# Kernel optimization log

Measured on AMD Instinct MI355X. Metric: run time of the kernel, lower is better.

Reference implementation:

```python
import jax, jax.numpy as jnp
import numpy as np
from math import sqrt

B, S, D, H = 4, 2048, 1024, 16
HD = D // H


def setup_inputs() -> dict:
    key = jax.random.key(0)
    ks = jax.random.split(key, 16)
    w = 0.02
    q = jax.random.normal(ks[0], (B, S, D), jnp.float32)
    k = jax.random.normal(ks[1], (B, S, D), jnp.float32)
    v = jax.random.normal(ks[2], (B, S, D), jnp.float32)
    # causal attention mask [1,1,S,S]
    attn_mask = jnp.tril(jnp.ones((S, S), jnp.int32))[None, None]
    # padding mask [B,1,1,S]; force position 0 valid so no softmax row is all -inf
    pad_mask = jax.random.randint(ks[3], (B, 1, 1, S), 0, 2, jnp.int32)
    pad_mask = pad_mask.at[..., 0].set(1)
    params = {
        'Wq': jax.random.normal(ks[4], (D, D), jnp.float32) * w,
        'bq': jnp.zeros((D,), jnp.float32),
        'Wk': jax.random.normal(ks[5], (D, D), jnp.float32) * w,
        'bk': jnp.zeros((D,), jnp.float32),
        'Wv': jax.random.normal(ks[6], (D, D), jnp.float32) * w,
        'bv': jnp.zeros((D,), jnp.float32),
        'Wo': jax.random.normal(ks[7], (D, D), jnp.float32) * w,
        'bo': jnp.zeros((D,), jnp.float32),
        'gamma': jnp.ones((D,), jnp.float32),
        'beta': jnp.zeros((D,), jnp.float32),
    }
    return dict(q=q, k=k, v=v, attn_mask=attn_mask, pad_mask=pad_mask, **params)


def _mha(q, k, v, Wq, bq, Wk, bk, Wv, bv, Wo, bo, gamma, beta, attn_mask, pad_mask):
    seq = q.shape[1]
    # residual path is detached in the original (q.clone().detach())
    x = jax.lax.stop_gradient(q)
    # Linear projections (torch Linear: y = x @ W.T + b)
    qp = (q @ Wq.T + bq).reshape(-1, H, seq, HD)   # raw view, NO head transpose (faithful)
    kp = (k @ Wk.T + bk).reshape(-1, H, seq, HD)
    vp = (v @ Wv.T + bv).reshape(-1, H, seq, HD)
    scores = jnp.einsum('bhqd,bhkd->bhqk', qp, kp)   # [B,H,S,S]
    scores = jnp.where(pad_mask == 0, -jnp.inf, scores)
    scores = jnp.where(attn_mask == 0, -jnp.inf, scores)
    # scaling applied AFTER masking, as in source
    attn = jax.nn.softmax(scores / sqrt(HD), axis=-1)
    out = jnp.einsum('bhqk,bhkd->bhqd', attn, vp).reshape(-1, seq, D)
    out = out @ Wo.T + bo  # dropout is identity in eval
    y = x + out
    mean = jnp.mean(y, axis=-1, keepdims=True)
    std = jnp.sqrt(jnp.mean((y - mean) ** 2, axis=-1, keepdims=True))
    return gamma * ((y - mean) / (std + 1e-8)) + beta


def reference(q, k, v, attn_mask, pad_mask, Wq, bq, Wk, bk, Wv, bv, Wo, bo, gamma, beta):
    return _mha(q, k, v, Wq, bq, Wk, bk, Wv, bv, Wo, bo, gamma, beta, attn_mask, pad_mask)
```

## Files before the change

kernel.cpp:

```cpp
#include <hip/hip_runtime.h>
#include <hip/hip_bf16.h>
#include <math.h>

#define B_  4
#define S_  2048
#define D_  1024
#define H_  16
#define HD_ 64
#define SD_  (S_*D_)
#define SHD_ (S_*HD_)

typedef __attribute__((ext_vector_type(8))) short          bf16x8;
typedef __attribute__((ext_vector_type(4))) float          f32x4;
typedef __attribute__((ext_vector_type(8))) unsigned short us8;
typedef __attribute__((ext_vector_type(4))) unsigned short us4;

__device__ __forceinline__ unsigned short f2bf(float x) {
  unsigned int u = __float_as_uint(x);
  u += 0x7fffu + ((u >> 16) & 1u);
  return (unsigned short)(u >> 16);
}
__device__ __forceinline__ float bf2f(unsigned short u) {
  return __uint_as_float(((unsigned int)u) << 16);
}

__device__ __forceinline__ void gload16(const unsigned short* g, unsigned short* l) {
  __builtin_amdgcn_global_load_lds(
      (const __attribute__((address_space(1))) unsigned int*)g,
      (__attribute__((address_space(3))) unsigned int*)l,
      16, 0, 0);
}

__device__ __forceinline__ void stage_swz(const unsigned short* __restrict__ g,
                                          int rstride ,
                                          unsigned short* lds, int tid)
{
#pragma unroll
  for (int rr = 0; rr < 2; ++rr) {
    const int cidx = tid + rr * 256;
    const int row  = cidx >> 3;
    const int sb   = ((cidx & 7) * 16) ^ ((row & 7) << 4);
    gload16(g + (size_t)row * rstride + (sb >> 1), lds + cidx * 8);
  }
}

__device__ __forceinline__ void read_frag_pair(const unsigned short* lds, int row,
                                               int quad, bf16x8& f0, bf16x8& f1)
{
  const int sw = (row & 7) << 4;
  const unsigned short* p = lds + row * 64;
  f0 = *(const bf16x8*)(p + (((quad * 16) ^ sw) >> 1));
  f1 = *(const bf16x8*)(p + (((64 + quad * 16) ^ sw) >> 1));
}

__global__ __launch_bounds__(256) void cvt_a(const float* __restrict__ s,
                                             unsigned short* __restrict__ d)
{
  int i = blockIdx.x * 256 + threadIdx.x;
  float4 v = ((const float4*)s)[i];
  us4 o = { f2bf(v.x), f2bf(v.y), f2bf(v.z), f2bf(v.w) };
  *(us4*)(d + (size_t)i * 4) = o;
}

__global__ __launch_bounds__(256) void cvt_w(const float* __restrict__ w0,
                                             const float* __restrict__ w1,
                                             const float* __restrict__ w2,
                                             const float* __restrict__ w3,
                                             unsigned short* __restrict__ dst)
{
  const float* s = (blockIdx.y == 0) ? w0 : (blockIdx.y == 1) ? w1
                 : (blockIdx.y == 2) ? w2 : w3;
  unsigned short* d = dst + (size_t)blockIdx.y * 1024 * 1024;
  int i = blockIdx.x * 256 + threadIdx.x;
  float4 v = ((const float4*)s)[i];
  us4 o = { f2bf(v.x), f2bf(v.y), f2bf(v.z), f2bf(v.w) };
  *(us4*)(d + (size_t)i * 4) = o;
}

__global__ __launch_bounds__(256) void pad_cvt(const int* __restrict__ pad,
                                               float* __restrict__ padf)
{
  int i = (blockIdx.x * 256 + threadIdx.x) * 4;
  int4 pv = *(const int4*)(pad + i);
  float4 o = { pv.x ? 0.f : -1e30f, pv.y ? 0.f : -1e30f,
               pv.z ? 0.f : -1e30f, pv.w ? 0.f : -1e30f };
  *(float4*)(padf + i) = o;
}

__global__ __launch_bounds__(256) void cvt_all(
    const float* __restrict__ q, const float* __restrict__ k,
    const float* __restrict__ v,
    const float* __restrict__ w0, const float* __restrict__ w1,
    const float* __restrict__ w2, const float* __restrict__ w3,
    const int* __restrict__ pad,
    unsigned short* __restrict__ Ac3, unsigned short* __restrict__ Wall,
    float* __restrict__ padf)
{
  const int bx = blockIdx.x;
  if (bx < 24576) {
    const int y = bx >> 13;
    const int i = (bx & 8191) * 256 + threadIdx.x;
    const float* s = (y == 0) ? q : (y == 1) ? k : v;
    unsigned short* d = Ac3 + (size_t)y * (B_ * (size_t)SD_);
    float4 x = ((const float4*)s)[i];
    us4 o = { f2bf(x.x), f2bf(x.y), f2bf(x.z), f2bf(x.w) };
    *(us4*)(d + (size_t)i * 4) = o;
  } else if (bx < 24576 + 4096) {
    const int bw = bx - 24576;
    const int y = bw >> 10;
    const int i = (bw & 1023) * 256 + threadIdx.x;
    const float* s = (y == 0) ? w0 : (y == 1) ? w1 : (y == 2) ? w2 : w3;
    unsigned short* d = Wall + (size_t)y * 1024 * 1024;
    float4 x = ((const float4*)s)[i];
    us4 o = { f2bf(x.x), f2bf(x.y), f2bf(x.z), f2bf(x.w) };
    *(us4*)(d + (size_t)i * 4) = o;
  } else {
    const int i = ((bx - 28672) * 256 + threadIdx.x) * 4;
    int4 pv = *(const int4*)(pad + i);
    float4 o = { pv.x ? 0.f : -1e30f, pv.y ? 0.f : -1e30f,
                 pv.z ? 0.f : -1e30f, pv.w ? 0.f : -1e30f };
    *(float4*)(padf + i) = o;
  }
}

__device__ __forceinline__ void gemm_body(
    const unsigned short* __restrict__ A,
    const unsigned short* __restrict__ Wb,
    const float* __restrict__ bias,
    unsigned short* __restrict__ Cb,
    int n0, int m0)
{
  __shared__ unsigned short As[2][128 * 32];
  __shared__ unsigned short Bs[2][128 * 32];

  const int tid  = threadIdx.x;
  const int lane = tid & 63;
  const int w    = tid >> 6;
  const int wm   = w >> 1, wn = w & 1;
  const int l16  = lane & 15, quad = lane >> 4;

  f32x4 acc[4][4];
#pragma unroll
  for (int mt = 0; mt < 4; ++mt)
#pragma unroll
    for (int nt = 0; nt < 4; ++nt) acc[mt][nt] = (f32x4){0.f, 0.f, 0.f, 0.f};

  const int srow = lane >> 2;
  const int sseg = (lane & 3) * 8;
  const int r0   = w * 32 + srow;

  const unsigned short* Ar0 = A  + (size_t)(m0 + r0) * 1024 + sseg;
  const unsigned short* Ar1 = A  + (size_t)(m0 + r0 + 16) * 1024 + sseg;
  const unsigned short* Br0 = Wb + (size_t)(n0 + r0) * 1024 + sseg;
  const unsigned short* Br1 = Wb + (size_t)(n0 + r0 + 16) * 1024 + sseg;

  auto STAGE = [&](int buf, int kt) {
    const int ko = kt * 32;
    gload16(Ar0 + ko, &As[buf][r0 * 32 + sseg]);
    gload16(Ar1 + ko, &As[buf][(r0 + 16) * 32 + sseg]);
    gload16(Br0 + ko, &Bs[buf][r0 * 32 + sseg]);
    gload16(Br1 + ko, &Bs[buf][(r0 + 16) * 32 + sseg]);
  };

  STAGE(0, 0);
  int cur = 0;
  for (int kt = 0; kt < 32; ++kt) {
    if (kt < 31) {
      STAGE(cur ^ 1, kt + 1);
      asm volatile("s_waitcnt vmcnt(4)" ::: "memory");
    } else {
      asm volatile("s_waitcnt vmcnt(0)" ::: "memory");
    }
    __builtin_amdgcn_sched_barrier(0);
    __builtin_amdgcn_s_barrier();

    bf16x8 af[4], bfr[4];
#pragma unroll
    for (int mt = 0; mt < 4; ++mt)
      af[mt] = *(const bf16x8*)&As[cur][(wm * 64 + mt * 16 + l16) * 32 + quad * 8];
#pragma unroll
    for (int nt = 0; nt < 4; ++nt)
      bfr[nt] = *(const bf16x8*)&Bs[cur][(wn * 64 + nt * 16 + l16) * 32 + quad * 8];
#pragma unroll
    for (int mt = 0; mt < 4; ++mt)
#pragma unroll
      for (int nt = 0; nt < 4; ++nt)
        acc[mt][nt] = __builtin_amdgcn_mfma_f32_16x16x32_bf16(
            af[mt], bfr[nt], acc[mt][nt], 0, 0, 0);

    __builtin_amdgcn_sched_barrier(0);
    __builtin_amdgcn_s_barrier();
    cur ^= 1;
  }

#pragma unroll
  for (int nt = 0; nt < 4; ++nt) {
    const int ncol = n0 + wn * 64 + nt * 16 + l16;
    const float bv = bias[ncol];
#pragma unroll
    for (int mt = 0; mt < 4; ++mt) {
      const int row = m0 + wm * 64 + mt * 16 + quad * 4;
#pragma unroll
      for (int reg = 0; reg < 4; ++reg)
        Cb[(size_t)(row + reg) * 1024 + ncol] = f2bf(acc[mt][nt][reg] + bv);
    }
  }
}

__device__ __forceinline__ void xcd_coords(int& n0, int& m0)
{
  const int nwgx = gridDim.x;
  const int nwg  = nwgx * gridDim.y;
  const int bid  = blockIdx.y * nwgx + blockIdx.x;
  const int sw   = (bid & 7) * (nwg >> 3) + (bid >> 3);
  n0 = (sw % nwgx) * 128;
  m0 = (sw / nwgx) * 128;
}

__global__ __launch_bounds__(256) void gemm_mfma(
    const unsigned short* __restrict__ A, const unsigned short* __restrict__ Wb,
    const float* __restrict__ bias, unsigned short* __restrict__ Cb)
{
  int n0, m0;
  xcd_coords(n0, m0);
  gemm_body(A, Wb, bias, Cb, n0, m0);
}

__global__ __launch_bounds__(256) void gemm_qkv(
    const unsigned short* __restrict__ A3,
    const unsigned short* __restrict__ Wall,
    const float* __restrict__ bq, const float* __restrict__ bk,
    const float* __restrict__ bv,
    unsigned short* __restrict__ Qb, unsigned short* __restrict__ Kb,
    unsigned short* __restrict__ Vb)
{
  const int z = blockIdx.z;
  const unsigned short* A  = A3 + (size_t)z * (B_ * (size_t)SD_);
  const unsigned short* Wb = Wall + (size_t)z * 1024 * 1024;
  const float* bias = (z == 0) ? bq : (z == 1) ? bk : bv;
  unsigned short* Cb = (z == 0) ? Qb : (z == 1) ? Kb : Vb;
  int n0, m0;
  xcd_coords(n0, m0);
  gemm_body(A, Wb, bias, Cb, n0, m0);
}

__global__ __launch_bounds__(256) void vtrans(
    const unsigned short* __restrict__ V, unsigned short* __restrict__ Vt)
{
  __shared__ unsigned short t[64][72];
  const int tid = threadIdx.x;
  const int st  = blockIdx.x;
  const int bh  = blockIdx.y;
  const unsigned short* src = V + (size_t)bh * SHD_ + (size_t)st * 4096;

#pragma unroll
  for (int u = tid; u < 512; u += 256) {
    us8 vv = ((const us8*)src)[u];
    int s  = u >> 3;
    int dg = (u & 7) * 8;
    *(us8*)&t[s][dg] = vv;
  }
  __syncthreads();

  unsigned short* dst = Vt + (size_t)bh * SHD_ + st * 64;
#pragma unroll
  for (int u = tid; u < 1024; u += 256) {
    int d  = u >> 4;
    int s4 = (u & 15) * 4;
    us4 o = { t[s4][d], t[s4 + 1][d], t[s4 + 2][d], t[s4 + 3][d] };
    *(us4*)(dst + (size_t)d * 2048 + s4) = o;
  }
}

__global__ __launch_bounds__(256, 4) void attn_mfma(
    unsigned short* __restrict__ Qb, const unsigned short* __restrict__ Kb,
    const unsigned short* __restrict__ Vt, const float* __restrict__ padf)
{
  __shared__ unsigned short Ks[64 * 64];
  __shared__ unsigned short Vs[2][64 * 64];
  __shared__ unsigned short Ps[4][16][72];

  const int tid  = threadIdx.x;
  const int lane = tid & 63;
  const int w    = tid >> 6;
  const int p    = blockIdx.x;
  const int bh   = blockIdx.y;
  const int b    = bh >> 4;
  const size_t base = (size_t)bh * SHD_;

  const int l16  = lane & 15;
  const int quad = lane >> 4;

  for (int half = 0; half < 2; ++half) {
    const int it = half ? (31 - p) : p;

    bf16x8 qfrag[2];
    {
      const unsigned short* qrow = Qb + base + (size_t)(it * 64 + w * 16 + l16) * 64;
      qfrag[0] = *(const bf16x8*)(qrow + quad * 8);
      qfrag[1] = *(const bf16x8*)(qrow + 32 + quad * 8);
    }

    f32x4 oacc[4];
#pragma unroll
    for (int dt = 0; dt < 4; ++dt) oacc[dt] = (f32x4){0.f, 0.f, 0.f, 0.f};
    float mS = -INFINITY, lS = 0.f;

    __syncthreads();
    stage_swz(Kb + base, 64, Ks, tid);
    stage_swz(Vt + base, 2048, Vs[0], tid);
    float4 pf[4];
#pragma unroll
    for (int ct = 0; ct < 4; ++ct)
      pf[ct] = *(const float4*)(padf + b * S_ + ct * 16 + quad * 4);
    int cur = 0;

    for (int jt = 0; jt <= it; ++jt) {
      __syncthreads();

      f32x4 sacc[4];
#pragma unroll
      for (int ct = 0; ct < 4; ++ct) {
        bf16x8 k0, k1;
        read_frag_pair(Ks, ct * 16 + l16, quad, k0, k1);
        f32x4 s = (f32x4){0.f, 0.f, 0.f, 0.f};
        s = __builtin_amdgcn_mfma_f32_16x16x32_bf16(k0, qfrag[0], s, 0, 0, 0);
        s = __builtin_amdgcn_mfma_f32_16x16x32_bf16(k1, qfrag[1], s, 0, 0, 0);
        sacc[ct] = s;
      }

      float4 pfn[4];
      if (jt < it) {
        __syncthreads();
        stage_swz(Kb + base + (size_t)(jt + 1) * 4096, 64, Ks, tid);
        stage_swz(Vt + base + (jt + 1) * 64, 2048, Vs[cur ^ 1], tid);
#pragma unroll
        for (int ct = 0; ct < 4; ++ct)
          pfn[ct] = *(const float4*)(padf + b * S_ + (jt + 1) * 64 + ct * 16 + quad * 4);
      }

      float lg[4][4];
      float mx = -INFINITY;
#pragma unroll
      for (int ct = 0; ct < 4; ++ct)
#pragma unroll
        for (int reg = 0; reg < 4; ++reg) {
          float sc = fmaf(sacc[ct][reg], 0.125f, ((const float*)&pf[ct])[reg]);
          if (jt == it) {
            bool ok = (ct * 16 + quad * 4 + reg) <= (w * 16 + l16);
            sc = ok ? sc : -1e30f;
          }
          lg[ct][reg] = sc;
          mx = fmaxf(mx, sc);
        }
      mx = fmaxf(mx, __shfl_xor(mx, 16, 64));
      mx = fmaxf(mx, __shfl_xor(mx, 32, 64));
      const float mnew = fmaxf(mS, mx);
      const float a    = __expf(mS - mnew);
      float sm = 0.f;
#pragma unroll
      for (int ct = 0; ct < 4; ++ct) {
        us4 pk;
#pragma unroll
        for (int reg = 0; reg < 4; ++reg) {
          float pe = __expf(lg[ct][reg] - mnew);
          sm += pe;
          pk[reg] = f2bf(pe);
        }
        *(us4*)&Ps[w][l16][ct * 16 + quad * 4] = pk;
      }
      sm += __shfl_xor(sm, 16, 64);
      sm += __shfl_xor(sm, 32, 64);
      lS = lS * a + sm;
      mS = mnew;

      float aO[4];
#pragma unroll
      for (int reg = 0; reg < 4; ++reg) aO[reg] = __shfl(a, quad * 4 + reg, 64);
#pragma unroll
      for (int dt = 0; dt < 4; ++dt)
#pragma unroll
        for (int reg = 0; reg < 4; ++reg) oacc[dt][reg] *= aO[reg];

      bf16x8 pfrag0 = *(const bf16x8*)&Ps[w][l16][quad * 8];
      bf16x8 pfrag1 = *(const bf16x8*)&Ps[w][l16][32 + quad * 8];
#pragma unroll
      for (int dt = 0; dt < 4; ++dt) {
        bf16x8 v0, v1;
        read_frag_pair(Vs[cur], dt * 16 + l16, quad, v0, v1);
        oacc[dt] = __builtin_amdgcn_mfma_f32_16x16x32_bf16(pfrag0, v0, oacc[dt], 0, 0, 0);
        oacc[dt] = __builtin_amdgcn_mfma_f32_16x16x32_bf16(pfrag1, v1, oacc[dt], 0, 0, 0);
      }

      if (jt < it) {
#pragma unroll
        for (int ct = 0; ct < 4; ++ct) pf[ct] = pfn[ct];
        cur ^= 1;
      }
    }

    float lO[4];
#pragma unroll
    for (int reg = 0; reg < 4; ++reg) lO[reg] = __shfl(lS, quad * 4 + reg, 64);
#pragma unroll
    for (int reg = 0; reg < 4; ++reg) {
      const float rl = 1.0f / lO[reg];
      unsigned short* orow = Qb + base + (size_t)(it * 64 + w * 16 + quad * 4 + reg) * 64;
#pragma unroll
      for (int dt = 0; dt < 4; ++dt)
        orow[dt * 16 + l16] = f2bf(oacc[dt][reg] * rl);
    }
  }
}

__global__ __launch_bounds__(256) void ln_kernel(
    const float* __restrict__ x, const unsigned short* __restrict__ O,
    const float* __restrict__ gamma, const float* __restrict__ beta,
    float* __restrict__ out)
{
  __shared__ float red[8];
  const int row = blockIdx.x;
  const int tid = threadIdx.x;
  float4 xv = ((const float4*)x)[(size_t)row * 256 + tid];
  us4 ov4 = *(const us4*)(O + (size_t)row * 1024 + tid * 4);
  float4 y = make_float4(xv.x + bf2f(ov4[0]), xv.y + bf2f(ov4[1]),
                         xv.z + bf2f(ov4[2]), xv.w + bf2f(ov4[3]));
  float s1 = y.x + y.y + y.z + y.w;
  float s2 = y.x*y.x + y.y*y.y + y.z*y.z + y.w*y.w;
#pragma unroll
  for (int off = 32; off >= 1; off >>= 1) {
    s1 += __shfl_xor(s1, off, 64);
    s2 += __shfl_xor(s2, off, 64);
  }
  if ((tid & 63) == 0) { red[tid >> 6] = s1; red[4 + (tid >> 6)] = s2; }
  __syncthreads();
  s1 = red[0] + red[1] + red[2] + red[3];
  s2 = red[4] + red[5] + red[6] + red[7];
  const float mean = s1 * (1.0f / 1024.0f);
  const float var  = fmaxf(s2 * (1.0f / 1024.0f) - mean * mean, 0.f);
  const float rstd = 1.0f / (sqrtf(var) + 1e-8f);
  float4 gv = ((const float4*)gamma)[tid];
  float4 bv = ((const float4*)beta)[tid];
  float4 r;
  r.x = gv.x * (y.x - mean) * rstd + bv.x;
  r.y = gv.y * (y.y - mean) * rstd + bv.y;
  r.z = gv.z * (y.z - mean) * rstd + bv.z;
  r.w = gv.w * (y.w - mean) * rstd + bv.w;
  ((float4*)out)[(size_t)row * 256 + tid] = r;
}

extern "C" void kernel_launch(void* const* d_in, const int* in_sizes, int n_in,
                              void* d_out, int out_size, void* d_ws, size_t ws_size,
                              hipStream_t stream)
{
  const float* q  = (const float*)d_in[0];
  const float* k  = (const float*)d_in[1];
  const float* v  = (const float*)d_in[2];
  const int*   pad = (const int*)d_in[4];
  const float* Wq = (const float*)d_in[5];
  const float* bq = (const float*)d_in[6];
  const float* Wk = (const float*)d_in[7];
  const float* bk = (const float*)d_in[8];
  const float* Wv = (const float*)d_in[9];
  const float* bv = (const float*)d_in[10];
  const float* Wo = (const float*)d_in[11];
  const float* bo = (const float*)d_in[12];
  const float* gamma = (const float*)d_in[13];
  const float* beta  = (const float*)d_in[14];
  float* out = (float*)d_out;

  char* ws = (char*)d_ws;
  const size_t MB = 1024 * 1024;
  dim3 gg(8, 64), bb(256);

  if (ws_size >= 121 * MB) {
    unsigned short* Ac3  = (unsigned short*)(ws);
    unsigned short* Qb   = (unsigned short*)(ws + 48 * MB);
    unsigned short* Kb   = (unsigned short*)(ws + 64 * MB);
    unsigned short* Vb   = (unsigned short*)(ws + 80 * MB);
    unsigned short* Vtb  = (unsigned short*)(ws + 96 * MB);
    unsigned short* Wall = (unsigned short*)(ws + 112 * MB);
    float*          padf = (float*)(ws + 120 * MB);
    unsigned short* Obuf = Ac3;

    cvt_all<<<dim3(28680), 256, 0, stream>>>(q, k, v, Wq, Wk, Wv, Wo, pad,
                                             Ac3, Wall, padf);
    gemm_qkv<<<dim3(8, 64, 3), bb, 0, stream>>>(Ac3, Wall, bq, bk, bv, Qb, Kb, Vb);
    vtrans<<<dim3(32, 64), 256, 0, stream>>>(Vb, Vtb);
    attn_mfma<<<dim3(16, 64), 256, 0, stream>>>(Qb, Kb, Vtb, padf);
    gemm_mfma<<<gg, bb, 0, stream>>>(Qb, Wall + 3 * MB, bo, Obuf);
    ln_kernel<<<dim3(B_ * S_), 256, 0, stream>>>(q, Obuf, gamma, beta, out);
  } else {
    unsigned short* Ac   = (unsigned short*)(ws);
    unsigned short* Qb   = (unsigned short*)(ws + 16 * MB);
    unsigned short* Kb   = (unsigned short*)(ws + 32 * MB);
    unsigned short* Vb   = (unsigned short*)(ws + 48 * MB);
    unsigned short* Vtb  = (unsigned short*)(ws + 64 * MB);
    unsigned short* Wall = (unsigned short*)(ws + 80 * MB);
    float*          padf = (float*)(ws + 88 * MB);
    unsigned short* Obuf = Ac;

    cvt_w<<<dim3(1024, 4), 256, 0, stream>>>(Wq, Wk, Wv, Wo, Wall);
    pad_cvt<<<8, 256, 0, stream>>>(pad, padf);
    cvt_a<<<8192, 256, 0, stream>>>(q, Ac);
    gemm_mfma<<<gg, bb, 0, stream>>>(Ac, Wall + 0 * MB, bq, Qb);
    cvt_a<<<8192, 256, 0, stream>>>(k, Ac);
    gemm_mfma<<<gg, bb, 0, stream>>>(Ac, Wall + 1 * MB, bk, Kb);
    cvt_a<<<8192, 256, 0, stream>>>(v, Ac);
    gemm_mfma<<<gg, bb, 0, stream>>>(Ac, Wall + 2 * MB, bv, Vb);
    vtrans<<<dim3(32, 64), 256, 0, stream>>>(Vb, Vtb);
    attn_mfma<<<dim3(16, 64), 256, 0, stream>>>(Qb, Kb, Vtb, padf);
    gemm_mfma<<<gg, bb, 0, stream>>>(Qb, Wall + 3 * MB, bo, Obuf);
    ln_kernel<<<dim3(B_ * S_), 256, 0, stream>>>(q, Obuf, gamma, beta, out);
  }
}
```

Baseline: 381.4 us.

## Swizzle GEMM LDS layout, remap attention blocks, and skip softmax rescale

The GEMM staging now uses an XOR-swizzled LDS layout and plain __syncthreads double buffering in place of explicit vmcnt waits, aiming to cut bank conflicts. The attention kernel remaps block ids so heads are spread across XCDs. Its online softmax skips the max update and output rescale unless some row's max exceeds the running max by more than 8, a lazy-rescale trick. That trick adds a wave-wide vote and lets exponent values grow up to e^8 before rescaling.

Measured after the change: 366.3 us. 1.04x faster.

```diff
diff --git a/kernel.cpp b/kernel.cpp
--- a/kernel.cpp
+++ b/kernel.cpp
@@ -123,6 +123,35 @@
   }
 }
 
+__device__ __forceinline__ void xcd_coords(int& n0, int& m0)
+{
+  const int nwgx = gridDim.x;
+  const int nwg  = nwgx * gridDim.y;
+  const int bid  = blockIdx.y * nwgx + blockIdx.x;
+  const int sw   = (bid & 7) * (nwg >> 3) + (bid >> 3);
+  n0 = (sw % nwgx) * 128;
+  m0 = (sw / nwgx) * 128;
+}
+
+__device__ __forceinline__ void gemm_epilogue(
+    f32x4 (&acc)[4][4], const float* __restrict__ bias,
+    unsigned short* __restrict__ Cb, int n0, int m0,
+    int wm, int wn, int l16, int quad)
+{
+#pragma unroll
+  for (int nt = 0; nt < 4; ++nt) {
+    const int ncol = n0 + wn * 64 + nt * 16 + l16;
+    const float bv = bias[ncol];
+#pragma unroll
+    for (int mt = 0; mt < 4; ++mt) {
+      const int row = m0 + wm * 64 + mt * 16 + quad * 4;
+#pragma unroll
+      for (int reg = 0; reg < 4; ++reg)
+        Cb[(size_t)(row + reg) * 1024 + ncol] = f2bf(acc[mt][nt][reg] + bv);
+    }
+  }
+}
+
 __device__ __forceinline__ void gemm_body(
     const unsigned short* __restrict__ A,
     const unsigned short* __restrict__ Wb,
@@ -130,8 +159,8 @@
     unsigned short* __restrict__ Cb,
     int n0, int m0)
 {
-  __shared__ unsigned short As[2][128 * 32];
-  __shared__ unsigned short Bs[2][128 * 32];
+  __shared__ unsigned short As[2][4096];
+  __shared__ unsigned short Bs[2][4096];
 
   const int tid  = threadIdx.x;
   const int lane = tid & 63;
@@ -145,42 +174,46 @@
 #pragma unroll
     for (int nt = 0; nt < 4; ++nt) acc[mt][nt] = (f32x4){0.f, 0.f, 0.f, 0.f};
 
-  const int srow = lane >> 2;
-  const int sseg = (lane & 3) * 8;
-  const int r0   = w * 32 + srow;
-
-  const unsigned short* Ar0 = A  + (size_t)(m0 + r0) * 1024 + sseg;
-  const unsigned short* Ar1 = A  + (size_t)(m0 + r0 + 16) * 1024 + sseg;
-  const unsigned short* Br0 = Wb + (size_t)(n0 + r0) * 1024 + sseg;
-  const unsigned short* Br1 = Wb + (size_t)(n0 + r0 + 16) * 1024 + sseg;
-
-  auto STAGE = [&](int buf, int kt) {
-    const int ko = kt * 32;
-    gload16(Ar0 + ko, &As[buf][r0 * 32 + sseg]);
-    gload16(Ar1 + ko, &As[buf][(r0 + 16) * 32 + sseg]);
-    gload16(Br0 + ko, &Bs[buf][r0 * 32 + sseg]);
-    gload16(Br1 + ko, &Bs[buf][(r0 + 16) * 32 + sseg]);
+  const int L0   = tid >> 3;
+  const int s0d  = (tid & 7) ^ (L0 & 7);
+  const int srw  = (L0 << 1) | (s0d & 1);
+  const int sc   = (s0d >> 1) * 8;
+
+  const unsigned short* A0 = A  + (size_t)(m0 + srw) * 1024 + sc;
+  const unsigned short* A1 = A  + (size_t)(m0 + srw + 64) * 1024 + sc;
+  const unsigned short* B0 = Wb + (size_t)(n0 + srw) * 1024 + sc;
+  const unsigned short* B1 = Wb + (size_t)(n0 + srw + 64) * 1024 + sc;
+  unsigned short* dA = &As[0][tid * 8];
+  unsigned short* dB = &Bs[0][tid * 8];
+
+  auto STAGE = [&](int buf, int ko) {
+    const int bo = buf * 4096;
+    gload16(A0 + ko, dA + bo);
+    gload16(A1 + ko, dA + bo + 2048);
+    gload16(B0 + ko, dB + bo);
+    gload16(B1 + ko, dB + bo + 2048);
   };
 
+  const int swz   = ((((quad << 1) | (l16 & 1)) ^ (l16 >> 1)) << 3);
+  const int rbA   = (wm * 32 + (l16 >> 1)) * 64 + swz;
+  const int rbB   = (wn * 32 + (l16 >> 1)) * 64 + swz;
+
   STAGE(0, 0);
-  int cur = 0;
+  int buf = 0;
   for (int kt = 0; kt < 32; ++kt) {
-    if (kt < 31) {
-      STAGE(cur ^ 1, kt + 1);
-      asm volatile("s_waitcnt vmcnt(4)" ::: "memory");
-    } else {
-      asm volatile("s_waitcnt vmcnt(0)" ::: "memory");
-    }
-    __builtin_amdgcn_sched_barrier(0);
-    __builtin_amdgcn_s_barrier();
-
+    __syncthreads();
+
+    if (kt < 31) STAGE(buf ^ 1, (kt + 1) * 32);
+
+    const unsigned short* Ab = As[buf];
+    const unsigned short* Bb = Bs[buf];
     bf16x8 af[4], bfr[4];
 #pragma unroll
     for (int mt = 0; mt < 4; ++mt)
-      af[mt] = *(const bf16x8*)&As[cur][(wm * 64 + mt * 16 + l16) * 32 + quad * 8];
+      af[mt] = *(const bf16x8*)&Ab[rbA + mt * 512];
 #pragma unroll
     for (int nt = 0; nt < 4; ++nt)
-      bfr[nt] = *(const bf16x8*)&Bs[cur][(wn * 64 + nt * 16 + l16) * 32 + quad * 8];
+      bfr[nt] = *(const bf16x8*)&Bb[rbB + nt * 512];
 #pragma unroll
     for (int mt = 0; mt < 4; ++mt)
 #pragma unroll
@@ -188,33 +221,10 @@
         acc[mt][nt] = __builtin_amdgcn_mfma_f32_16x16x32_bf16(
             af[mt], bfr[nt], acc[mt][nt], 0, 0, 0);
 
-    __builtin_amdgcn_sched_barrier(0);
-    __builtin_amdgcn_s_barrier();
-    cur ^= 1;
-  }
-
-#pragma unroll
-  for (int nt = 0; nt < 4; ++nt) {
-    const int ncol = n0 + wn * 64 + nt * 16 + l16;
-    const float bv = bias[ncol];
-#pragma unroll
-    for (int mt = 0; mt < 4; ++mt) {
-      const int row = m0 + wm * 64 + mt * 16 + quad * 4;
-#pragma unroll
-      for (int reg = 0; reg < 4; ++reg)
-        Cb[(size_t)(row + reg) * 1024 + ncol] = f2bf(acc[mt][nt][reg] + bv);
-    }
-  }
-}
-
-__device__ __forceinline__ void xcd_coords(int& n0, int& m0)
-{
-  const int nwgx = gridDim.x;
-  const int nwg  = nwgx * gridDim.y;
-  const int bid  = blockIdx.y * nwgx + blockIdx.x;
-  const int sw   = (bid & 7) * (nwg >> 3) + (bid >> 3);
-  n0 = (sw % nwgx) * 128;
-  m0 = (sw / nwgx) * 128;
+    buf ^= 1;
+  }
+
+  gemm_epilogue(acc, bias, Cb, n0, m0, wm, wn, l16, quad);
 }
 
 __global__ __launch_bounds__(256) void gemm_mfma(
@@ -283,8 +293,9 @@
   const int tid  = threadIdx.x;
   const int lane = tid & 63;
   const int w    = tid >> 6;
-  const int p    = blockIdx.x;
-  const int bh   = blockIdx.y;
+  const int id   = blockIdx.y * 16 + blockIdx.x;
+  const int p    = id >> 6;
+  const int bh   = (id & 7) + 8 * ((id >> 3) & 7);
   const int b    = bh >> 4;
   const size_t base = (size_t)bh * SHD_;
 
@@ -355,15 +366,28 @@
         }
       mx = fmaxf(mx, __shfl_xor(mx, 16, 64));
       mx = fmaxf(mx, __shfl_xor(mx, 32, 64));
-      const float mnew = fmaxf(mS, mx);
-      const float a    = __expf(mS - mnew);
+
+      if (!__all(mx <= mS + 8.f)) {
+        const float mnew = fmaxf(mS, mx);
+        const float a    = __expf(mS - mnew);
+        mS = mnew;
+        lS *= a;
+        float aO[4];
+#pragma unroll
+        for (int reg = 0; reg < 4; ++reg) aO[reg] = __shfl(a, quad * 4 + reg, 64);
+#pragma unroll
+        for (int dt = 0; dt < 4; ++dt)
+#pragma unroll
+          for (int reg = 0; reg < 4; ++reg) oacc[dt][reg] *= aO[reg];
+      }
+
       float sm = 0.f;
 #pragma unroll
       for (int ct = 0; ct < 4; ++ct) {
         us4 pk;
 #pragma unroll
         for (int reg = 0; reg < 4; ++reg) {
-          float pe = __expf(lg[ct][reg] - mnew);
+          float pe = __expf(lg[ct][reg] - mS);
           sm += pe;
           pk[reg] = f2bf(pe);
         }
@@ -371,16 +395,7 @@
       }
       sm += __shfl_xor(sm, 16, 64);
       sm += __shfl_xor(sm, 32, 64);
-      lS = lS * a + sm;
-      mS = mnew;
-
-      float aO[4];
-#pragma unroll
-      for (int reg = 0; reg < 4; ++reg) aO[reg] = __shfl(a, quad * 4 + reg, 64);
-#pragma unroll
-      for (int dt = 0; dt < 4; ++dt)
-#pragma unroll
-        for (int reg = 0; reg < 4; ++reg) oacc[dt][reg] *= aO[reg];
+      lS += sm;
 
       bf16x8 pfrag0 = *(const bf16x8*)&Ps[w][l16][quad * 8];
       bf16x8 pfrag1 = *(const bf16x8*)&Ps[w][l16][32 + quad * 8];
```
